# Optimization experiments

Hardware: AMD Instinct MI355X
Metric: run time of the kernel (lower is better)

Reference implementation:

```python
import jax, jax.numpy as jnp
import numpy as np

N_TAGS = 128
ROOT = 126
END = 127
NEG = -10000.0


def setup_inputs() -> dict:
    key = jax.random.key(0)
    k1, k2, k3, k4 = jax.random.split(key, 4)
    bsz, T = 256, 256
    feats = jax.random.normal(k1, (bsz, T, N_TAGS), jnp.float32)
    tags = jax.random.randint(k2, (bsz, T), 0, ROOT)  # never ROOT/END
    lengths = jax.random.randint(k3, (bsz,), 1, T + 1)
    mask = (jnp.arange(T)[None, :] < lengths[:, None]).astype(jnp.int32)
    # xavier_normal_: std = gain * sqrt(2 / (fan_in + fan_out))
    std = np.float32(np.sqrt(2.0 / (2 * N_TAGS)))
    lt = jax.random.normal(k4, (N_TAGS, N_TAGS), jnp.float32) * std
    lt = lt.at[:, ROOT].set(NEG).at[END, :].set(NEG)
    return {"feats": feats, "tags": tags, "mask": mask, "log_transitions": lt}


def _neg_log_likelihood(feats, log_transitions, tags, maskf):
    bsz, T, n = feats.shape
    # ---- forward belief propagation (log partition) ----
    init = log_transitions[ROOT, :] + feats[:, 0, :]  # [b, n]

    def step(fv, xs):
        feat, m = xs  # feat: [b, n], m: [b]
        # logsumexp over previous tag axis; emission is independent of it
        nxt = jax.nn.logsumexp(fv[:, :, None] + log_transitions[None, :, :], axis=1) + feat
        return jnp.where(m[:, None] > 0, nxt, fv), None

    feats_t = jnp.swapaxes(feats, 0, 1)  # [T, b, n]
    fv, _ = jax.lax.scan(step, init, (feats_t[1:], maskf[:, 1:].T))
    partition = jax.nn.logsumexp(fv + log_transitions[:, END][None, :], axis=1)  # [b]

    # ---- gold path score ----
    trans_tt = log_transitions[tags[:, :-1], tags[:, 1:]]                         # [b, T-1]
    emis = jnp.take_along_axis(feats[:, :-1, :], tags[:, :-1, None], axis=2)[..., 0]
    scores = log_transitions[ROOT, tags[:, 0]]
    scores = scores + jnp.sum(trans_tt * maskf[:, 1:] + emis * maskf[:, :-1], axis=1)
    last_idx = (maskf.sum(axis=1) - 1.0).astype(jnp.int32)                         # [b]
    last_tags = jnp.take_along_axis(tags, last_idx[:, None], axis=1)[:, 0]
    last_input = jnp.take_along_axis(feats[:, -1, :], last_tags[:, None], axis=1)[:, 0]
    scores = scores + log_transitions[last_tags, END] + last_input * maskf[:, -1]

    return jnp.mean(partition - scores)


def reference(feats, tags, mask, log_transitions):
    maskf = mask.astype(feats.dtype)
    return _neg_log_likelihood(feats, log_transitions, tags, maskf)
```

## Files before the change

kernel.cpp:

```cpp
#include <hip/hip_runtime.h>
#include <hip/hip_bf16.h>

#define N_TAGS 128
#define T_LEN  256
#define BSZ    256
#define ROOT_T 126
#define END_T  127

typedef _Float16 h2 __attribute__((ext_vector_type(2)));
typedef _Float16 h8 __attribute__((ext_vector_type(8)));
typedef int   i32x4 __attribute__((ext_vector_type(4)));

static __device__ __forceinline__ h2 pkrtz(float a, float b) {
  return __builtin_bit_cast(h2, __builtin_amdgcn_cvt_pkrtz(a, b));
}

static __device__ __forceinline__ float rfl(float x) {
  return __int_as_float(__builtin_amdgcn_readfirstlane(__float_as_int(x)));
}

static __device__ __forceinline__ float fdot2(h2 a, h2 b, float c) {
#if __has_builtin(__builtin_amdgcn_fdot2)
  return __builtin_amdgcn_fdot2(a, b, c, false);
#else
  float d;
  asm("v_dot2_f32_f16 %0, %1, %2, %3" : "=v"(d) : "v"(a), "v"(b), "v"(c));
  return d;
#endif
}

static __device__ __forceinline__ float wave_max(float x) {
  #pragma unroll
  for (int d = 1; d < 64; d <<= 1) x = fmaxf(x, __shfl_xor(x, d));
  return x;
}

static __device__ __forceinline__ void dot128(const h2* __restrict__ psv,
                                              const h2 (&EA)[64], const h2 (&EB)[64],
                                              float& s0, float& s1) {
  const h8* pv = (const h8*)psv;
  float a0=0.f,a1=0.f,a2=0.f,a3=0.f, b0=0.f,b1=0.f,b2=0.f,b3=0.f;
  #pragma unroll
  for (int r = 0; r < 16; ++r) {
    const h8 v = pv[r];
    const h2 p0 = __builtin_shufflevector(v, v, 0, 1);
    const h2 p1 = __builtin_shufflevector(v, v, 2, 3);
    const h2 p2 = __builtin_shufflevector(v, v, 4, 5);
    const h2 p3 = __builtin_shufflevector(v, v, 6, 7);
    a0 = fdot2(p0, EA[4*r+0], a0);  a1 = fdot2(p1, EA[4*r+1], a1);
    a2 = fdot2(p2, EA[4*r+2], a2);  a3 = fdot2(p3, EA[4*r+3], a3);
    b0 = fdot2(p0, EB[4*r+0], b0);  b1 = fdot2(p1, EB[4*r+1], b1);
    b2 = fdot2(p2, EB[4*r+2], b2);  b3 = fdot2(p3, EB[4*r+3], b3);
  }
  s0 = (a0 + a1) + (a2 + a3);
  s1 = (b0 + b1) + (b2 + b3);
}

__global__ void
__attribute__((amdgpu_flat_work_group_size(128, 128), amdgpu_waves_per_eu(1, 1)))
crf_fwd_kernel(
    const float* __restrict__ feats,
    const int*   __restrict__ tags,
    const int*   __restrict__ mask,
    const float* __restrict__ lt,
    float*       __restrict__ per_batch)
{
  const int b    = blockIdx.x;
  const int tid  = threadIdx.x;
  const int lane = tid & 63;
  const int wave = tid >> 6;

  __shared__ __align__(16) h2 psF[2][64];
  __shared__ __align__(16) h2 psB[2][64];
  __shared__ float stage[32 * 129];
  __shared__ float bb[N_TAGS];
  __shared__ float sred[2];

  const float* fb = feats + (size_t)b * T_LEN * N_TAGS;
  const int*   tb = tags  + b * T_LEN;

  int len;
  {
    const i32x4 mv = ((const i32x4*)(mask + b * T_LEN))[lane];
    int v = mv.x + mv.y + mv.z + mv.w;
    #pragma unroll
    for (int d = 1; d < 64; d <<= 1) v += __shfl_xor(v, d);
    len = __builtin_amdgcn_readfirstlane(v);
  }

  h2 EA[64], EB[64];
  #pragma unroll
  for (int c = 0; c < 4; ++c) {
    __syncthreads();
    #pragma unroll
    for (int rr = 0; rr < 32; ++rr)
      stage[rr * 129 + tid] = __expf(lt[(c * 32 + rr) * N_TAGS + tid]);
    __syncthreads();
    if (wave == 0) {
      #pragma unroll
      for (int k = 0; k < 16; ++k) {
        h2 ea, eb;
        ea.x = (_Float16)stage[(2*k)   * 129 + 2*lane];
        ea.y = (_Float16)stage[(2*k+1) * 129 + 2*lane];
        eb.x = (_Float16)stage[(2*k)   * 129 + 2*lane + 1];
        eb.y = (_Float16)stage[(2*k+1) * 129 + 2*lane + 1];
        EA[c*16 + k] = ea;
        EB[c*16 + k] = eb;
      }
    } else if ((lane >> 4) == c) {
      const int r0 = 2 * lane - 32 * c;
      #pragma unroll
      for (int q = 0; q < 64; ++q) {
        h2 ea, eb;
        ea.x = (_Float16)stage[r0       * 129 + 2*q];
        ea.y = (_Float16)stage[r0       * 129 + 2*q + 1];
        eb.x = (_Float16)stage[(r0 + 1) * 129 + 2*q];
        eb.y = (_Float16)stage[(r0 + 1) * 129 + 2*q + 1];
        EA[q] = ea;
        EB[q] = eb;
      }
    }
  }

  float st0, st1;

  if (wave == 0) {
    {
      const float2 f0 = ((const float2*)fb)[lane];
      st0 = lt[ROOT_T * N_TAGS + 2*lane]     + f0.x;
      st1 = lt[ROOT_T * N_TAGS + 2*lane + 1] + f0.y;
    }
    float2 fa = ((const float2*)(fb + 1 * N_TAGS))[lane];
    float2 fc = ((const float2*)(fb + 2 * N_TAGS))[lane];
    float m_cur = rfl(st0) + 2.0f;
    psF[1][lane] = pkrtz(__expf(st0 - m_cur), __expf(st1 - m_cur));

    #pragma unroll 1
    for (int k2 = 0; k2 < 64; ++k2) {
      {
        const int t = 2 * k2 + 1;
        float s0, s1; dot128(psF[1], EA, EB, s0, s1);
        const float nf0 = m_cur + __logf(s0) + fa.x;
        const float nf1 = m_cur + __logf(s1) + fa.y;
        const bool act = (t < len);
        st0 = act ? nf0 : st0;  st1 = act ? nf1 : st1;
        fa = fc;
        fc = ((const float2*)(fb + (t + 2) * N_TAGS))[lane];
        const float m = rfl(st0) + 2.0f;
        psF[0][lane] = pkrtz(__expf(st0 - m), __expf(st1 - m));
        m_cur = m;
      }
      {
        const int t = 2 * k2 + 2;
        float s0, s1; dot128(psF[0], EA, EB, s0, s1);
        const float nf0 = m_cur + __logf(s0) + fa.x;
        const float nf1 = m_cur + __logf(s1) + fa.y;
        const bool act = (t < len);
        st0 = act ? nf0 : st0;  st1 = act ? nf1 : st1;
        fa = fc;
        fc = ((const float2*)(fb + (t + 2) * N_TAGS))[lane];
        const float m = rfl(st0) + 2.0f;
        psF[1][lane] = pkrtz(__expf(st0 - m), __expf(st1 - m));
        m_cur = m;
      }
    }
  } else {
    st0 = lt[(2*lane)     * N_TAGS + END_T];
    st1 = lt[(2*lane + 1) * N_TAGS + END_T];
    float2 fw = ((const float2*)(fb + 255 * N_TAGS))[lane];
    float2 fa = ((const float2*)(fb + 254 * N_TAGS))[lane];
    float2 fc = ((const float2*)(fb + 253 * N_TAGS))[lane];
    const float y0i = st0 + fw.x, y1i = st1 + fw.y;
    float m_cur = rfl(y0i) + 2.0f;
    psB[1][lane] = pkrtz(__expf(y0i - m_cur), __expf(y1i - m_cur));

    const int kmin = 256 - len;
    #pragma unroll 1
    for (int k2 = 0; k2 < 64; ++k2) {
      {
        const int k = 2 * k2;
        float s0, s1; dot128(psB[1], EA, EB, s0, s1);
        const float nb0 = m_cur + __logf(s0);
        const float nb1 = m_cur + __logf(s1);
        const bool act = (k >= kmin) && (k <= 126);
        st0 = act ? nb0 : st0;  st1 = act ? nb1 : st1;
        const float w0 = fa.x, w1 = fa.y;
        fa = fc;
        fc = ((const float2*)(fb + (252 - k) * N_TAGS))[lane];
        const float y0 = st0 + w0, y1 = st1 + w1;
        const float m = rfl(y0) + 2.0f;
        psB[0][lane] = pkrtz(__expf(y0 - m), __expf(y1 - m));
        m_cur = m;
      }
      {
        const int k = 2 * k2 + 1;
        float s0, s1; dot128(psB[0], EA, EB, s0, s1);
        const float nb0 = m_cur + __logf(s0);
        const float nb1 = m_cur + __logf(s1);
        const bool act = (k >= kmin) && (k <= 126);
        st0 = act ? nb0 : st0;  st1 = act ? nb1 : st1;
        const float w0 = fa.x, w1 = fa.y;
        fa = fc;
        fc = ((const float2*)(fb + (252 - k) * N_TAGS))[lane];
        const float y0 = st0 + w0, y1 = st1 + w1;
        const float m = rfl(y0) + 2.0f;
        psB[1][lane] = pkrtz(__expf(y0 - m), __expf(y1 - m));
        m_cur = m;
      }
    }
    bb[2*lane]     = st0;
    bb[2*lane + 1] = st1;
  }
  __syncthreads();

  float c = 0.f;
  #pragma unroll
  for (int q = 0; q < 2; ++q) {
    const int t  = tid + q * N_TAGS;
    const int tg = tb[t];
    if (t == 0)                           c += lt[ROOT_T * N_TAGS + tg];
    if (t >= 1 && t < len)                c += lt[tb[t - 1] * N_TAGS + tg];
    if (t < len && t <= T_LEN - 2)        c += fb[t * N_TAGS + tg];
    if (t == len - 1)                     c += lt[tg * N_TAGS + END_T];
    if (t == T_LEN - 1 && len == T_LEN)   c += fb[t * N_TAGS + tg];
  }
  #pragma unroll
  for (int d = 1; d < 64; d <<= 1) c += __shfl_xor(c, d);
  if (lane == 0) sred[wave] = c;

  float part = 0.f;
  if (wave == 0) {
    const float x0 = st0 + bb[2*lane];
    const float x1 = st1 + bb[2*lane + 1];
    const float mw = wave_max(fmaxf(x0, x1));
    float e = __expf(x0 - mw) + __expf(x1 - mw);
    #pragma unroll
    for (int d = 1; d < 64; d <<= 1) e += __shfl_xor(e, d);
    part = mw + __logf(e);
  }
  __syncthreads();

  if (tid == 0) per_batch[b] = part - (sred[0] + sred[1]);
}

__global__ __launch_bounds__(256) void crf_reduce_kernel(
    const float* __restrict__ per_batch, float* __restrict__ out)
{
  const int tid = threadIdx.x;
  float v = per_batch[tid] * (1.0f / BSZ);
  #pragma unroll
  for (int d = 1; d < 64; d <<= 1) v += __shfl_xor(v, d);
  __shared__ float r[4];
  if ((tid & 63) == 0) r[tid >> 6] = v;
  __syncthreads();
  if (tid == 0) out[0] = r[0] + r[1] + r[2] + r[3];
}

extern "C" void kernel_launch(void* const* d_in, const int* in_sizes, int n_in,
                              void* d_out, int out_size, void* d_ws, size_t ws_size,
                              hipStream_t stream) {
  (void)in_sizes; (void)n_in; (void)out_size; (void)ws_size;
  const float* feats = (const float*)d_in[0];
  const int*   tags  = (const int*)d_in[1];
  const int*   mask  = (const int*)d_in[2];
  const float* lt    = (const float*)d_in[3];
  float* per_batch = (float*)d_ws;

  crf_fwd_kernel<<<BSZ, 128, 0, stream>>>(feats, tags, mask, lt, per_batch);
  crf_reduce_kernel<<<1, 256, 0, stream>>>(per_batch, (float*)d_out);
}
```

Baseline: 74.60 us.

## Process two batch elements per block sharing register-resident transition matrix

Each block now handles two batch rows, interleaving their forward and backward recurrences in the same waves so the exp(transition) registers are reused and two independent dependency chains hide latency. The grid is halved to 128 blocks. This should amortize the transition setup and fill stalls in the serial logsumexp chain. The cost is fewer blocks than the 256 CUs on MI355X, so half the device sits idle, and each step's instruction count roughly doubles.

```diff
diff --git a/kernel.cpp b/kernel.cpp
--- a/kernel.cpp
+++ b/kernel.cpp
@@ -14,11 +14,9 @@
 static __device__ __forceinline__ h2 pkrtz(float a, float b) {
   return __builtin_bit_cast(h2, __builtin_amdgcn_cvt_pkrtz(a, b));
 }
-
 static __device__ __forceinline__ float rfl(float x) {
   return __int_as_float(__builtin_amdgcn_readfirstlane(__float_as_int(x)));
 }
-
 static __device__ __forceinline__ float fdot2(h2 a, h2 b, float c) {
 #if __has_builtin(__builtin_amdgcn_fdot2)
   return __builtin_amdgcn_fdot2(a, b, c, false);
@@ -28,7 +26,6 @@
   return d;
 #endif
 }
-
 static __device__ __forceinline__ float wave_max(float x) {
   #pragma unroll
   for (int d = 1; d < 64; d <<= 1) x = fmaxf(x, __shfl_xor(x, d));
@@ -65,27 +62,33 @@
     const float* __restrict__ lt,
     float*       __restrict__ per_batch)
 {
-  const int b    = blockIdx.x;
+  const int b0   = 2 * blockIdx.x;
+  const int b1   = b0 + 1;
   const int tid  = threadIdx.x;
   const int lane = tid & 63;
   const int wave = tid >> 6;
 
-  __shared__ __align__(16) h2 psF[2][64];
-  __shared__ __align__(16) h2 psB[2][64];
+  __shared__ __align__(16) h2 psF[2][2][64];
+  __shared__ __align__(16) h2 psB[2][2][64];
   __shared__ float stage[32 * 129];
-  __shared__ float bb[N_TAGS];
-  __shared__ float sred[2];
-
-  const float* fb = feats + (size_t)b * T_LEN * N_TAGS;
-  const int*   tb = tags  + b * T_LEN;
-
-  int len;
+  __shared__ float bbs[2][N_TAGS];
+  __shared__ float sred[2][2];
+
+  const float* fb0 = feats + (size_t)b0 * T_LEN * N_TAGS;
+  const float* fb1 = feats + (size_t)b1 * T_LEN * N_TAGS;
+  const int*   tb0 = tags + b0 * T_LEN;
+  const int*   tb1 = tags + b1 * T_LEN;
+
+  int lenA, lenB;
   {
-    const i32x4 mv = ((const i32x4*)(mask + b * T_LEN))[lane];
-    int v = mv.x + mv.y + mv.z + mv.w;
+    const i32x4 mvA = ((const i32x4*)(mask + b0 * T_LEN))[lane];
+    const i32x4 mvB = ((const i32x4*)(mask + b1 * T_LEN))[lane];
+    int vA = mvA.x + mvA.y + mvA.z + mvA.w;
+    int vB = mvB.x + mvB.y + mvB.z + mvB.w;
     #pragma unroll
-    for (int d = 1; d < 64; d <<= 1) v += __shfl_xor(v, d);
-    len = __builtin_amdgcn_readfirstlane(v);
+    for (int d = 1; d < 64; d <<= 1) { vA += __shfl_xor(vA, d); vB += __shfl_xor(vB, d); }
+    lenA = __builtin_amdgcn_readfirstlane(vA);
+    lenB = __builtin_amdgcn_readfirstlane(vB);
   }
 
   h2 EA[64], EB[64];
@@ -122,125 +125,171 @@
     }
   }
 
-  float st0, st1;
+  float sA0, sA1, sB0, sB1;
 
   if (wave == 0) {
     {
-      const float2 f0 = ((const float2*)fb)[lane];
-      st0 = lt[ROOT_T * N_TAGS + 2*lane]     + f0.x;
-      st1 = lt[ROOT_T * N_TAGS + 2*lane + 1] + f0.y;
-    }
-    float2 fa = ((const float2*)(fb + 1 * N_TAGS))[lane];
-    float2 fc = ((const float2*)(fb + 2 * N_TAGS))[lane];
-    float m_cur = rfl(st0) + 2.0f;
-    psF[1][lane] = pkrtz(__expf(st0 - m_cur), __expf(st1 - m_cur));
+      const float2 fA = ((const float2*)fb0)[lane];
+      const float2 fB = ((const float2*)fb1)[lane];
+      const float r0 = lt[ROOT_T * N_TAGS + 2*lane];
+      const float r1 = lt[ROOT_T * N_TAGS + 2*lane + 1];
+      sA0 = r0 + fA.x;  sA1 = r1 + fA.y;
+      sB0 = r0 + fB.x;  sB1 = r1 + fB.y;
+    }
+    float2 faA = ((const float2*)(fb0 + 1 * N_TAGS))[lane];
+    float2 fcA = ((const float2*)(fb0 + 2 * N_TAGS))[lane];
+    float2 faB = ((const float2*)(fb1 + 1 * N_TAGS))[lane];
+    float2 fcB = ((const float2*)(fb1 + 2 * N_TAGS))[lane];
+    float mA = rfl(sA0) + 2.0f;
+    float mB = rfl(sB0) + 2.0f;
+    psF[0][1][lane] = pkrtz(__expf(sA0 - mA), __expf(sA1 - mA));
+    psF[1][1][lane] = pkrtz(__expf(sB0 - mB), __expf(sB1 - mB));
 
     #pragma unroll 1
     for (int k2 = 0; k2 < 64; ++k2) {
-      {
-        const int t = 2 * k2 + 1;
-        float s0, s1; dot128(psF[1], EA, EB, s0, s1);
-        const float nf0 = m_cur + __logf(s0) + fa.x;
-        const float nf1 = m_cur + __logf(s1) + fa.y;
-        const bool act = (t < len);
-        st0 = act ? nf0 : st0;  st1 = act ? nf1 : st1;
-        fa = fc;
-        fc = ((const float2*)(fb + (t + 2) * N_TAGS))[lane];
-        const float m = rfl(st0) + 2.0f;
-        psF[0][lane] = pkrtz(__expf(st0 - m), __expf(st1 - m));
-        m_cur = m;
+      #pragma unroll
+      for (int h = 0; h < 2; ++h) {
+        const int t  = 2 * k2 + 1 + h;
+        const int rb = 1 - h, wb = h;
+        float d0A, d1A, d0B, d1B;
+        dot128(psF[0][rb], EA, EB, d0A, d1A);
+        dot128(psF[1][rb], EA, EB, d0B, d1B);
+        {
+          const float nf0 = mA + __logf(d0A) + faA.x;
+          const float nf1 = mA + __logf(d1A) + faA.y;
+          const bool act = (t < lenA);
+          sA0 = act ? nf0 : sA0;  sA1 = act ? nf1 : sA1;
+          faA = fcA;
+          fcA = ((const float2*)(fb0 + (t + 2) * N_TAGS))[lane];
+          const float m = rfl(sA0) + 2.0f;
+          psF[0][wb][lane] = pkrtz(__expf(sA0 - m), __expf(sA1 - m));
+          mA = m;
+        }
+        {
+          const float nf0 = mB + __logf(d0B) + faB.x;
+          const float nf1 = mB + __logf(d1B) + faB.y;
+          const bool act = (t < lenB);
+          sB0 = act ? nf0 : sB0;  sB1 = act ? nf1 : sB1;
+          faB = fcB;
+          fcB = ((const float2*)(fb1 + (t + 2) * N_TAGS))[lane];
+          const float m = rfl(sB0) + 2.0f;
+          psF[1][wb][lane] = pkrtz(__expf(sB0 - m), __expf(sB1 - m));
+          mB = m;
+        }
       }
-      {
-        const int t = 2 * k2 + 2;
-        float s0, s1; dot128(psF[0], EA, EB, s0, s1);
-        const float nf0 = m_cur + __logf(s0) + fa.x;
-        const float nf1 = m_cur + __logf(s1) + fa.y;
-        const bool act = (t < len);
-        st0 = act ? nf0 : st0;  st1 = act ? nf1 : st1;
-        fa = fc;
-        fc = ((const float2*)(fb + (t + 2) * N_TAGS))[lane];
-        const float m = rfl(st0) + 2.0f;
-        psF[1][lane] = pkrtz(__expf(st0 - m), __expf(st1 - m));
-        m_cur = m;
-      }
     }
   } else {
-    st0 = lt[(2*lane)     * N_TAGS + END_T];
-    st1 = lt[(2*lane + 1) * N_TAGS + END_T];
-    float2 fw = ((const float2*)(fb + 255 * N_TAGS))[lane];
-    float2 fa = ((const float2*)(fb + 254 * N_TAGS))[lane];
-    float2 fc = ((const float2*)(fb + 253 * N_TAGS))[lane];
-    const float y0i = st0 + fw.x, y1i = st1 + fw.y;
-    float m_cur = rfl(y0i) + 2.0f;
-    psB[1][lane] = pkrtz(__expf(y0i - m_cur), __expf(y1i - m_cur));
-
-    const int kmin = 256 - len;
+    {
+      const float e0 = lt[(2*lane)     * N_TAGS + END_T];
+      const float e1 = lt[(2*lane + 1) * N_TAGS + END_T];
+      sA0 = e0;  sA1 = e1;
+      sB0 = e0;  sB1 = e1;
+    }
+    float2 fwA = ((const float2*)(fb0 + 255 * N_TAGS))[lane];
+    float2 faA = ((const float2*)(fb0 + 254 * N_TAGS))[lane];
+    float2 fcA = ((const float2*)(fb0 + 253 * N_TAGS))[lane];
+    float2 fwB = ((const float2*)(fb1 + 255 * N_TAGS))[lane];
+    float2 faB = ((const float2*)(fb1 + 254 * N_TAGS))[lane];
+    float2 fcB = ((const float2*)(fb1 + 253 * N_TAGS))[lane];
+    const float yA0i = sA0 + fwA.x, yA1i = sA1 + fwA.y;
+    const float yB0i = sB0 + fwB.x, yB1i = sB1 + fwB.y;
+    float mA = rfl(yA0i) + 2.0f;
+    float mB = rfl(yB0i) + 2.0f;
+    psB[0][1][lane] = pkrtz(__expf(yA0i - mA), __expf(yA1i - mA));
+    psB[1][1][lane] = pkrtz(__expf(yB0i - mB), __expf(yB1i - mB));
+
+    const int kminA = 256 - lenA;
+    const int kminB = 256 - lenB;
     #pragma unroll 1
     for (int k2 = 0; k2 < 64; ++k2) {
-      {
-        const int k = 2 * k2;
-        float s0, s1; dot128(psB[1], EA, EB, s0, s1);
-        const float nb0 = m_cur + __logf(s0);
-        const float nb1 = m_cur + __logf(s1);
-        const bool act = (k >= kmin) && (k <= 126);
-        st0 = act ? nb0 : st0;  st1 = act ? nb1 : st1;
-        const float w0 = fa.x, w1 = fa.y;
-        fa = fc;
-        fc = ((const float2*)(fb + (252 - k) * N_TAGS))[lane];
-        const float y0 = st0 + w0, y1 = st1 + w1;
-        const float m = rfl(y0) + 2.0f;
-        psB[0][lane] = pkrtz(__expf(y0 - m), __expf(y1 - m));
-        m_cur = m;
+      #pragma unroll
+      for (int h = 0; h < 2; ++h) {
+        const int k  = 2 * k2 + h;
+        const int rb = 1 - h, wb = h;
+        float d0A, d1A, d0B, d1B;
+        dot128(psB[0][rb], EA, EB, d0A, d1A);
+        dot128(psB[1][rb], EA, EB, d0B, d1B);
+        {
+          const float nb0 = mA + __logf(d0A);
+          const float nb1 = mA + __logf(d1A);
+          const bool act = (k >= kminA) && (k <= 126);
+          sA0 = act ? nb0 : sA0;  sA1 = act ? nb1 : sA1;
+          const float w0 = faA.x, w1 = faA.y;
+          faA = fcA;
+          fcA = ((const float2*)(fb0 + (252 - k) * N_TAGS))[lane];
+          const float y0 = sA0 + w0, y1 = sA1 + w1;
+          const float m = rfl(y0) + 2.0f;
+          psB[0][wb][lane] = pkrtz(__expf(y0 - m), __expf(y1 - m));
+          mA = m;
+        }
+        {
+          const float nb0 = mB + __logf(d0B);
+          const float nb1 = mB + __logf(d1B);
+          const bool act = (k >= kminB) && (k <= 126);
+          sB0 = act ? nb0 : sB0;  sB1 = act ? nb1 : sB1;
+          const float w0 = faB.x, w1 = faB.y;
+          faB = fcB;
+          fcB = ((const float2*)(fb1 + (252 - k) * N_TAGS))[lane];
+          const float y0 = sB0 + w0, y1 = sB1 + w1;
+          const float m = rfl(y0) + 2.0f;
+          psB[1][wb][lane] = pkrtz(__expf(y0 - m), __expf(y1 - m));
+          mB = m;
+        }
       }
-      {
-        const int k = 2 * k2 + 1;
-        float s0, s1; dot128(psB[0], EA, EB, s0, s1);
-        const float nb0 = m_cur + __logf(s0);
-        const float nb1 = m_cur + __logf(s1);
-        const bool act = (k >= kmin) && (k <= 126);
-        st0 = act ? nb0 : st0;  st1 = act ? nb1 : st1;
-        const float w0 = fa.x, w1 = fa.y;
-        fa = fc;
-        fc = ((const float2*)(fb + (252 - k) * N_TAGS))[lane];
-        const float y0 = st0 + w0, y1 = st1 + w1;
-        const float m = rfl(y0) + 2.0f;
-        psB[1][lane] = pkrtz(__expf(y0 - m), __expf(y1 - m));
-        m_cur = m;
-      }
-    }
-    bb[2*lane]     = st0;
-    bb[2*lane + 1] = st1;
+    }
+    bbs[0][2*lane] = sA0;  bbs[0][2*lane + 1] = sA1;
+    bbs[1][2*lane] = sB0;  bbs[1][2*lane + 1] = sB1;
   }
   __syncthreads();
 
-  float c = 0.f;
+  float cA = 0.f, cB = 0.f;
   #pragma unroll
   for (int q = 0; q < 2; ++q) {
-    const int t  = tid + q * N_TAGS;
-    const int tg = tb[t];
-    if (t == 0)                           c += lt[ROOT_T * N_TAGS + tg];
-    if (t >= 1 && t < len)                c += lt[tb[t - 1] * N_TAGS + tg];
-    if (t < len && t <= T_LEN - 2)        c += fb[t * N_TAGS + tg];
-    if (t == len - 1)                     c += lt[tg * N_TAGS + END_T];
-    if (t == T_LEN - 1 && len == T_LEN)   c += fb[t * N_TAGS + tg];
-  }
-  #pragma unroll
-  for (int d = 1; d < 64; d <<= 1) c += __shfl_xor(c, d);
-  if (lane == 0) sred[wave] = c;
-
-  float part = 0.f;
+    const int t = tid + q * N_TAGS;
+    {
+      const int tg = tb0[t];
+      if (t == 0)                           cA += lt[ROOT_T * N_TAGS + tg];
+      if (t >= 1 && t < lenA)               cA += lt[tb0[t - 1] * N_TAGS + tg];
+      if (t < lenA && t <= T_LEN - 2)       cA += fb0[t * N_TAGS + tg];
+      if (t == lenA - 1)                    cA += lt[tg * N_TAGS + END_T];
+      if (t == T_LEN - 1 && lenA == T_LEN)  cA += fb0[t * N_TAGS + tg];
+    }
+    {
+      const int tg = tb1[t];
+      if (t == 0)                           cB += lt[ROOT_T * N_TAGS + tg];
+      if (t >= 1 && t < lenB)               cB += lt[tb1[t - 1] * N_TAGS + tg];
+      if (t < lenB && t <= T_LEN - 2)       cB += fb1[t * N_TAGS + tg];
+      if (t == lenB - 1)                    cB += lt[tg * N_TAGS + END_T];
+      if (t == T_LEN - 1 && lenB == T_LEN)  cB += fb1[t * N_TAGS + tg];
+    }
+  }
+  #pragma unroll
+  for (int d = 1; d < 64; d <<= 1) { cA += __shfl_xor(cA, d); cB += __shfl_xor(cB, d); }
+  if (lane == 0) { sred[0][wave] = cA; sred[1][wave] = cB; }
+
+  float partA = 0.f, partB = 0.f;
   if (wave == 0) {
-    const float x0 = st0 + bb[2*lane];
-    const float x1 = st1 + bb[2*lane + 1];
-    const float mw = wave_max(fmaxf(x0, x1));
-    float e = __expf(x0 - mw) + __expf(x1 - mw);
+    const float xA0 = sA0 + bbs[0][2*lane], xA1 = sA1 + bbs[0][2*lane + 1];
+    const float xB0 = sB0 + bbs[1][2*lane], xB1 = sB1 + bbs[1][2*lane + 1];
+    float mwA = fmaxf(xA0, xA1), mwB = fmaxf(xB0, xB1);
     #pragma unroll
-    for (int d = 1; d < 64; d <<= 1) e += __shfl_xor(e, d);
-    part = mw + __logf(e);
+    for (int d = 1; d < 64; d <<= 1) {
+      mwA = fmaxf(mwA, __shfl_xor(mwA, d));
+      mwB = fmaxf(mwB, __shfl_xor(mwB, d));
+    }
+    float eA = __expf(xA0 - mwA) + __expf(xA1 - mwA);
+    float eB = __expf(xB0 - mwB) + __expf(xB1 - mwB);
+    #pragma unroll
+    for (int d = 1; d < 64; d <<= 1) { eA += __shfl_xor(eA, d); eB += __shfl_xor(eB, d); }
+    partA = mwA + __logf(eA);
+    partB = mwB + __logf(eB);
   }
   __syncthreads();
 
-  if (tid == 0) per_batch[b] = part - (sred[0] + sred[1]);
+  if (tid == 0) {
+    per_batch[b0] = partA - (sred[0][0] + sred[0][1]);
+    per_batch[b1] = partB - (sred[1][0] + sred[1][1]);
+  }
 }
 
 __global__ __launch_bounds__(256) void crf_reduce_kernel(
@@ -266,6 +315,6 @@
   const float* lt    = (const float*)d_in[3];
   float* per_batch = (float*)d_ws;
 
-  crf_fwd_kernel<<<BSZ, 128, 0, stream>>>(feats, tags, mask, lt, per_batch);
+  crf_fwd_kernel<<<BSZ / 2, 128, 0, stream>>>(feats, tags, mask, lt, per_batch);
   crf_reduce_kernel<<<1, 256, 0, stream>>>(per_batch, (float*)d_out);
 }
```

Result: slower. 211.0 us (+182.8%).
